# Optimization experiments

Measured on AMD Instinct MI355X. Metric: run time of the kernel, lower is better.

Reference implementation:

```python
import jax, jax.numpy as jnp
import numpy as np

D_IN = 1024
D_OUT = 1024
NUM_HEADS = 16
HEAD_DIM = D_OUT // NUM_HEADS


def setup_inputs() -> dict:
    key = jax.random.key(0)
    k_x, k_qkv, k_pw, k_pb = jax.random.split(key, 4)
    x = jax.random.normal(k_x, (2, 2048, D_IN), dtype=jnp.float32)
    # torch nn.Linear(d_in, 3*d_out, bias=False): weight [3*d_out, d_in]
    w_qkv = jax.random.normal(k_qkv, (3 * D_OUT, D_IN), dtype=jnp.float32) * (1.0 / np.sqrt(D_IN))
    # proj: nn.Linear(d_out, d_out) with bias
    w_proj = jax.random.normal(k_pw, (D_OUT, D_OUT), dtype=jnp.float32) * (1.0 / np.sqrt(D_OUT))
    b_proj = jax.random.normal(k_pb, (D_OUT,), dtype=jnp.float32) * 0.01
    return {"x": x, "w_qkv": w_qkv, "w_proj": w_proj, "b_proj": b_proj}


def reference(x, w_qkv, w_proj, b_proj):
    B, S, _ = x.shape
    # fused QKV projection: [B,S,3*D_OUT]
    qkv = jnp.einsum('bsd,ed->bse', x, w_qkv)
    qkv = qkv.reshape(B, S, 3, NUM_HEADS, HEAD_DIM)
    q, k, v = jnp.moveaxis(qkv, 2, 0)  # each [B,S,H,Dh]
    scale = 1.0 / jnp.sqrt(jnp.asarray(HEAD_DIM, dtype=x.dtype))
    # scores [B,H,S,S]
    scores = jnp.einsum('bqhd,bkhd->bhqk', q, k) * scale
    causal = jnp.tril(jnp.ones((S, S), dtype=bool))
    scores = jnp.where(causal, scores, jnp.asarray(-jnp.inf, dtype=scores.dtype))
    attn = jax.nn.softmax(scores, axis=-1)
    ctx = jnp.einsum('bhqk,bkhd->bqhd', attn, v)  # [B,S,H,Dh]
    ctx = ctx.reshape(B, S, D_OUT)
    return jnp.einsum('bsd,ed->bse', ctx, w_proj) + b_proj
```

## Files before the change

kernel.cpp:

```cpp
#include <hip/hip_runtime.h>
#include <hip/hip_bf16.h>
#include <cstdint>

#define B_SZ   2
#define S_LEN  2048
#define NH     16
#define NT     32
#define LDA    72

using f32x4 = __attribute__((ext_vector_type(4))) float;
typedef __bf16 bf16x8 __attribute__((ext_vector_type(8)));
typedef __bf16 bf16x4 __attribute__((ext_vector_type(4)));

__device__ inline float bf2f(unsigned short u) {
    union { unsigned int i; float f; } v; v.i = ((unsigned int)u) << 16; return v.f;
}
__device__ inline unsigned short f2bf(float f) {
    union { float f; unsigned int i; } v; v.f = f;
    unsigned int r = v.i + 0x7fff + ((v.i >> 16) & 1);
    return (unsigned short)(r >> 16);
}
__device__ inline f32x4 mfma16(bf16x8 a, bf16x8 b, f32x4 c) {
    return __builtin_amdgcn_mfma_f32_16x16x32_bf16(a, b, c, 0, 0, 0);
}
__device__ inline void stC(float* C, size_t idx, float v)  { C[idx] = v; }
__device__ inline void stC(__bf16* C, size_t idx, float v) { ((unsigned short*)C)[idx] = f2bf(v); }

__global__ __launch_bounds__(256) void f2b2_kernel(
    const float* __restrict__ a, int na4, __bf16* __restrict__ outa,
    const float* __restrict__ b, int nb4, __bf16* __restrict__ outb)
{
    int i = blockIdx.x * blockDim.x + threadIdx.x;
    const float* src; __bf16* dst; int idx;
    if (i < na4)           { src = a; dst = outa; idx = i; }
    else if (i < na4 + nb4){ src = b; dst = outb; idx = i - na4; }
    else return;
    float4 v = ((const float4*)src)[idx];
    ushort4 o;
    o.x = f2bf(v.x); o.y = f2bf(v.y); o.z = f2bf(v.z); o.w = f2bf(v.w);
    ((ushort4*)dst)[idx] = o;
}

__global__ __launch_bounds__(256) void f2b_kernel(
    const float* __restrict__ in, __bf16* __restrict__ out, int n4)
{
    int i = blockIdx.x * blockDim.x + threadIdx.x;
    if (i < n4) {
        float4 v = ((const float4*)in)[i];
        ushort4 o;
        o.x = f2bf(v.x); o.y = f2bf(v.y); o.z = f2bf(v.z); o.w = f2bf(v.w);
        ((ushort4*)out)[i] = o;
    }
}

template <typename TO, int HAS_BIAS>
__global__ __launch_bounds__(256) void gemm128(
    const __bf16* __restrict__ A, const __bf16* __restrict__ W,
    const float* __restrict__ bias, TO* __restrict__ C,
    int M, int N, int K)
{
    __shared__ __bf16 Alds[2][128 * 32];
    __shared__ __bf16 Blds[2][128 * 32];
    const int tid  = threadIdx.x, lane = tid & 63, w = tid >> 6;
    const int c16  = lane & 15, quad = lane >> 4;
    const int mBase = blockIdx.y * 128, nBase = blockIdx.x * 128;
    const int moff = (w & 1) * 64, noff = (w >> 1) * 64;

    f32x4 acc[4][4];
#pragma unroll
    for (int i = 0; i < 4; ++i)
#pragma unroll
        for (int j = 0; j < 4; ++j) acc[i][j] = (f32x4){0.f, 0.f, 0.f, 0.f};

    auto stage = [&](int buf, int k0) {
#pragma unroll
        for (int p = 0; p < 2; ++p) {
            const int linear = p * 256 + tid;
            const int row = linear >> 2;
            const int seg = (linear & 3) ^ (row & 3);
            const int lbase = (p * 256 + w * 64) * 8;
            const __bf16* ga = A + (size_t)(mBase + row) * K + k0 + seg * 8;
            const __bf16* gb = W + (size_t)(nBase + row) * K + k0 + seg * 8;
            __builtin_amdgcn_global_load_lds(
                (const __attribute__((address_space(1))) void*)ga,
                (__attribute__((address_space(3))) void*)(&Alds[buf][lbase]), 16, 0, 0);
            __builtin_amdgcn_global_load_lds(
                (const __attribute__((address_space(1))) void*)gb,
                (__attribute__((address_space(3))) void*)(&Blds[buf][lbase]), 16, 0, 0);
        }
    };

    stage(0, 0);
    int cur = 0;
    for (int k0 = 0; k0 < K; k0 += 32) {
        __syncthreads();
        if (k0 + 32 < K) stage(cur ^ 1, k0 + 32);

        bf16x8 af[4], bw[4];
#pragma unroll
        for (int i = 0; i < 4; ++i) {
            const int rowA = moff + i * 16 + c16;
            af[i] = *(const bf16x8*)&Alds[cur][rowA * 32 + ((quad ^ (rowA & 3)) << 3)];
            const int rowB = noff + i * 16 + c16;
            bw[i] = *(const bf16x8*)&Blds[cur][rowB * 32 + ((quad ^ (rowB & 3)) << 3)];
        }
#pragma unroll
        for (int i = 0; i < 4; ++i)
#pragma unroll
            for (int j = 0; j < 4; ++j)
                acc[i][j] = mfma16(af[i], bw[j], acc[i][j]);
        cur ^= 1;
    }

#pragma unroll
    for (int j = 0; j < 4; ++j) {
        const int col = nBase + noff + j * 16 + c16;
        const float bv = HAS_BIAS ? bias[col] : 0.f;
#pragma unroll
        for (int i = 0; i < 4; ++i)
#pragma unroll
            for (int r = 0; r < 4; ++r) {
                const int row = mBase + moff + i * 16 + quad * 4 + r;
                stC(C, (size_t)row * N + col, acc[i][j][r] + bv);
            }
    }
}

template <typename TO, int HAS_BIAS>
__global__ __launch_bounds__(256) void gemm64(
    const __bf16* __restrict__ A, const __bf16* __restrict__ W,
    const float* __restrict__ bias, TO* __restrict__ C,
    int M, int N, int K)
{
    __shared__ __bf16 Alds[2][64 * 32];
    __shared__ __bf16 Blds[2][128 * 32];
    const int tid  = threadIdx.x, lane = tid & 63, w = tid >> 6;
    const int c16  = lane & 15, quad = lane >> 4;
    const int mBase = blockIdx.y * 64, nBase = blockIdx.x * 128;
    const int moff = (w & 1) * 32, noff = (w >> 1) * 64;

    f32x4 acc[2][4];
#pragma unroll
    for (int i = 0; i < 2; ++i)
#pragma unroll
        for (int j = 0; j < 4; ++j) acc[i][j] = (f32x4){0.f, 0.f, 0.f, 0.f};

    auto stage = [&](int buf, int k0) {
        {
            const int row = tid >> 2;
            const int seg = (tid & 3) ^ (row & 3);
            const int lbase = (w * 64) * 8;
            const __bf16* ga = A + (size_t)(mBase + row) * K + k0 + seg * 8;
            __builtin_amdgcn_global_load_lds(
                (const __attribute__((address_space(1))) void*)ga,
                (__attribute__((address_space(3))) void*)(&Alds[buf][lbase]), 16, 0, 0);
        }
#pragma unroll
        for (int p = 0; p < 2; ++p) {
            const int linear = p * 256 + tid;
            const int row = linear >> 2;
            const int seg = (linear & 3) ^ (row & 3);
            const int lbase = (p * 256 + w * 64) * 8;
            const __bf16* gb = W + (size_t)(nBase + row) * K + k0 + seg * 8;
            __builtin_amdgcn_global_load_lds(
                (const __attribute__((address_space(1))) void*)gb,
                (__attribute__((address_space(3))) void*)(&Blds[buf][lbase]), 16, 0, 0);
        }
    };

    stage(0, 0);
    int cur = 0;
    for (int k0 = 0; k0 < K; k0 += 32) {
        __syncthreads();
        if (k0 + 32 < K) stage(cur ^ 1, k0 + 32);

        bf16x8 af[2], bw[4];
#pragma unroll
        for (int i = 0; i < 2; ++i) {
            const int rowA = moff + i * 16 + c16;
            af[i] = *(const bf16x8*)&Alds[cur][rowA * 32 + ((quad ^ (rowA & 3)) << 3)];
        }
#pragma unroll
        for (int j = 0; j < 4; ++j) {
            const int rowB = noff + j * 16 + c16;
            bw[j] = *(const bf16x8*)&Blds[cur][rowB * 32 + ((quad ^ (rowB & 3)) << 3)];
        }
#pragma unroll
        for (int i = 0; i < 2; ++i)
#pragma unroll
            for (int j = 0; j < 4; ++j)
                acc[i][j] = mfma16(af[i], bw[j], acc[i][j]);
        cur ^= 1;
    }

#pragma unroll
    for (int j = 0; j < 4; ++j) {
        const int col = nBase + noff + j * 16 + c16;
        const float bv = HAS_BIAS ? bias[col] : 0.f;
#pragma unroll
        for (int i = 0; i < 2; ++i)
#pragma unroll
            for (int r = 0; r < 4; ++r) {
                const int row = mBase + moff + i * 16 + quad * 4 + r;
                stC(C, (size_t)row * N + col, acc[i][j][r] + bv);
            }
    }
}

__device__ __forceinline__ void attn_tile(
    const __bf16* __restrict__ qkv, __bf16* __restrict__ ctx,
    int b, int h, int qt, int tid,
    __bf16* Qs, __bf16* Ks, __bf16* Vs, __bf16* Ps)
{
    const int lane = tid & 63;
    const int w    = tid >> 6;
    const int c16  = lane & 15;
    const int quad = lane >> 4;
    const int qBase = qt * 64;

    const float QS = 0.125f * 1.4426950408889634f;

    const int krow0 = tid >> 3;
    const int kd0   = (tid & 7) * 8;
    const int c16t = tid & 15;
    const int jh   = (tid >> 4) & 1;
    const int dblk = tid >> 5;

    const size_t rowB = (size_t)b * S_LEN;
    const __bf16* kp0 = qkv + (rowB + krow0) * 3072 + 1024 + h * 64 + kd0;
    const __bf16* kp1 = kp0 + (size_t)32 * 3072;
    const __bf16* vp0 = qkv + (rowB + 2 * jh * 16 + c16t) * 3072 + 2048 + h * 64 + dblk * 8;
    const __bf16* vp1 = vp0 + (size_t)16 * 3072;

    uint4 kr0 = *(const uint4*)kp0;
    uint4 kr1 = *(const uint4*)kp1;
    uint4 vr0 = *(const uint4*)vp0;
    uint4 vr1 = *(const uint4*)vp1;

#pragma unroll
    for (int p = 0; p < 2; ++p) {
        const int linear = p * 256 + tid;
        const int row = linear >> 3;
        const int d0 = (linear & 7) * 8;
        const __bf16* g = qkv + (rowB + qBase + row) * 3072 + h * 64 + d0;
        uint4 raw = *(const uint4*)g;
        const unsigned short* u = (const unsigned short*)&raw;
        unsigned short tmp[8];
#pragma unroll
        for (int jj = 0; jj < 8; ++jj) tmp[jj] = f2bf(bf2f(u[jj]) * QS);
        *(uint4*)&Qs[row * LDA + d0] = *(const uint4*)tmp;
    }
    __syncthreads();

    const bf16x8 aq0 = *(const bf16x8*)&Qs[(w * 16 + c16) * LDA + quad * 8];
    const bf16x8 aq1 = *(const bf16x8*)&Qs[(w * 16 + c16) * LDA + 32 + quad * 8];

    float l_r[4] = {0.f, 0.f, 0.f, 0.f};
    f32x4 acc_o[4];
#pragma unroll
    for (int j = 0; j < 4; ++j) acc_o[j] = (f32x4){0.f, 0.f, 0.f, 0.f};

    const int nCh = qt + 1;
    for (int cc = 0; cc < nCh; ++cc) {
        *(uint4*)&Ks[krow0 * LDA + kd0]        = kr0;
        *(uint4*)&Ks[(krow0 + 32) * LDA + kd0] = kr1;
        {
            const unsigned short* e1 = (const unsigned short*)&vr0;
            const unsigned short* e2 = (const unsigned short*)&vr1;
#pragma unroll
            for (int d = 0; d < 8; ++d) {
                const unsigned pack = (unsigned)e1[d] | ((unsigned)e2[d] << 16);
                *(unsigned*)&Vs[(dblk * 8 + d) * LDA + c16t * 4 + 2 * jh] = pack;
            }
        }
        __syncthreads();

        if (cc + 1 < nCh) {
            kp0 += (size_t)64 * 3072; kp1 += (size_t)64 * 3072;
            vp0 += (size_t)64 * 3072; vp1 += (size_t)64 * 3072;
            kr0 = *(const uint4*)kp0;
            kr1 = *(const uint4*)kp1;
            vr0 = *(const uint4*)vp0;
            vr1 = *(const uint4*)vp1;
        }

        f32x4 sc[4];
#pragma unroll
        for (int j = 0; j < 4; ++j) sc[j] = (f32x4){0.f, 0.f, 0.f, 0.f};
#pragma unroll
        for (int j = 0; j < 4; ++j) {
            bf16x8 bk0 = *(const bf16x8*)&Ks[(j * 16 + c16) * LDA + quad * 8];
            bf16x8 bk1 = *(const bf16x8*)&Ks[(j * 16 + c16) * LDA + 32 + quad * 8];
            sc[j] = mfma16(aq0, bk0, sc[j]);
            sc[j] = mfma16(aq1, bk1, sc[j]);
        }

        if (cc == nCh - 1) {
#pragma unroll
            for (int j = 0; j < 4; ++j) {
                const int key = cc * 64 + j * 16 + c16;
#pragma unroll
                for (int r = 0; r < 4; ++r) {
                    const int q = qBase + w * 16 + quad * 4 + r;
                    if (key > q) sc[j][r] = -1e30f;
                }
            }
        }

        float p_[4][4];
#pragma unroll
        for (int j = 0; j < 4; ++j)
#pragma unroll
            for (int r = 0; r < 4; ++r)
                p_[j][r] = exp2f(sc[j][r]);
#pragma unroll
        for (int r = 0; r < 4; ++r)
            l_r[r] += (p_[0][r] + p_[1][r]) + (p_[2][r] + p_[3][r]);

#pragma unroll
        for (int r = 0; r < 4; ++r) {
            bf16x4 pb;
            pb[0] = (__bf16)p_[0][r]; pb[1] = (__bf16)p_[1][r];
            pb[2] = (__bf16)p_[2][r]; pb[3] = (__bf16)p_[3][r];
            *(bf16x4*)&Ps[(w * 16 + quad * 4 + r) * LDA + c16 * 4] = pb;
        }

        bf16x8 ap0 = *(const bf16x8*)&Ps[(w * 16 + c16) * LDA + quad * 8];
        bf16x8 ap1 = *(const bf16x8*)&Ps[(w * 16 + c16) * LDA + 32 + quad * 8];
#pragma unroll
        for (int j = 0; j < 4; ++j) {
            bf16x8 bv0 = *(const bf16x8*)&Vs[(j * 16 + c16) * LDA + quad * 8];
            bf16x8 bv1 = *(const bf16x8*)&Vs[(j * 16 + c16) * LDA + 32 + quad * 8];
            acc_o[j] = mfma16(ap0, bv0, acc_o[j]);
            acc_o[j] = mfma16(ap1, bv1, acc_o[j]);
        }
        __syncthreads();
    }

#pragma unroll
    for (int r = 0; r < 4; ++r) {
        float l = l_r[r];
        l += __shfl_xor(l, 1);
        l += __shfl_xor(l, 2);
        l += __shfl_xor(l, 4);
        l += __shfl_xor(l, 8);
        const float inv = 1.0f / l;
        const size_t rowO = (rowB + qBase + w * 16 + quad * 4 + r) * 1024 + h * 64;
#pragma unroll
        for (int j = 0; j < 4; ++j)
            ctx[rowO + j * 16 + c16] = (__bf16)(acc_o[j][r] * inv);
    }
}

__global__ __launch_bounds__(256) void attn(
    const __bf16* __restrict__ qkv, __bf16* __restrict__ ctx)
{
    __shared__ __bf16 Qs[64 * LDA];
    __shared__ __bf16 Ks[64 * LDA];
    __shared__ __bf16 Vs[64 * LDA];
    __shared__ __bf16 Ps[64 * LDA];

    const int bh = blockIdx.x, b = bh >> 4, h = bh & 15;
    const int y  = blockIdx.y;

    attn_tile(qkv, ctx, b, h, NT - 1 - y, threadIdx.x, Qs, Ks, Vs, Ps);
    attn_tile(qkv, ctx, b, h, y,          threadIdx.x, Qs, Ks, Vs, Ps);
}

extern "C" void kernel_launch(void* const* d_in, const int* in_sizes, int n_in,
                              void* d_out, int out_size, void* d_ws, size_t ws_size,
                              hipStream_t stream) {
    const float* x      = (const float*)d_in[0];
    const float* w_qkv  = (const float*)d_in[1];
    const float* w_proj = (const float*)d_in[2];
    const float* b_proj = (const float*)d_in[3];
    float* out = (float*)d_out;

    __bf16* qkvb = (__bf16*)d_ws;
    __bf16* xb   = qkvb + (size_t)4096 * 3072;
    __bf16* wqb  = xb + (size_t)4096 * 1024;
    __bf16* ctxb = xb;
    __bf16* wpb  = wqb;

    const int M = B_SZ * S_LEN;
    const int nx4 = 4096 * 1024 / 4, nq4 = 3072 * 1024 / 4, np4 = 1024 * 1024 / 4;

    f2b2_kernel<<<(nx4 + nq4 + 255) / 256, 256, 0, stream>>>(x, nx4, xb, w_qkv, nq4, wqb);

    gemm128<__bf16, 0><<<dim3(3072 / 128, M / 128), 256, 0, stream>>>(
        xb, wqb, nullptr, qkvb, M, 3072, 1024);

    f2b_kernel<<<(np4 + 255) / 256, 256, 0, stream>>>(w_proj, wpb, np4);

    attn<<<dim3(B_SZ * NH, NT / 2), 256, 0, stream>>>(qkvb, ctxb);

    gemm64<float, 1><<<dim3(1024 / 128, M / 64), 256, 0, stream>>>(
        ctxb, wpb, b_proj, out, M, 1024, 1024);
}
```

Before: 190.9 us.

## Split long causal attention rows into two KV segments with combine kernel

```diff
diff --git a/kernel.cpp b/kernel.cpp
--- a/kernel.cpp
+++ b/kernel.cpp
@@ -207,16 +207,30 @@
     }
 }
 
-__device__ __forceinline__ void attn_tile(
+__global__ __launch_bounds__(256) void attn(
     const __bf16* __restrict__ qkv, __bf16* __restrict__ ctx,
-    int b, int h, int qt, int tid,
-    __bf16* Qs, __bf16* Ks, __bf16* Vs, __bf16* Ps)
-{
+    float* __restrict__ opart, float* __restrict__ lpart)
+{
+    __shared__ __bf16 Qs[64 * LDA];
+    __shared__ __bf16 Ks[64 * LDA];
+    __shared__ __bf16 Vs[64 * LDA];
+    __shared__ __bf16 Ps[64 * LDA];
+
+    const int tid  = threadIdx.x;
     const int lane = tid & 63;
     const int w    = tid >> 6;
     const int c16  = lane & 15;
     const int quad = lane >> 4;
+    const int bh = blockIdx.x, b = bh >> 4, h = bh & 15;
+    const int y  = blockIdx.y;
+
+    int qt, c0, c1, seg;
+    bool split;
+    if (y < 16)      { qt = 16 + y; const int half = (qt + 2) >> 1; c0 = 0;    c1 = half;   split = true;  seg = 0; }
+    else if (y < 32) { qt = y;      const int half = (qt + 2) >> 1; c0 = half; c1 = qt + 1; split = true;  seg = 1; }
+    else             { qt = 47 - y; c0 = 0; c1 = qt + 1; split = false; seg = 0; }
     const int qBase = qt * 64;
+    const int segIdx = split ? ((bh * 16 + (qt - 16)) * 2 + seg) : 0;
 
     const float QS = 0.125f * 1.4426950408889634f;
 
@@ -227,9 +241,9 @@
     const int dblk = tid >> 5;
 
     const size_t rowB = (size_t)b * S_LEN;
-    const __bf16* kp0 = qkv + (rowB + krow0) * 3072 + 1024 + h * 64 + kd0;
+    const __bf16* kp0 = qkv + (rowB + c0 * 64 + krow0) * 3072 + 1024 + h * 64 + kd0;
     const __bf16* kp1 = kp0 + (size_t)32 * 3072;
-    const __bf16* vp0 = qkv + (rowB + 2 * jh * 16 + c16t) * 3072 + 2048 + h * 64 + dblk * 8;
+    const __bf16* vp0 = qkv + (rowB + c0 * 64 + 2 * jh * 16 + c16t) * 3072 + 2048 + h * 64 + dblk * 8;
     const __bf16* vp1 = vp0 + (size_t)16 * 3072;
 
     uint4 kr0 = *(const uint4*)kp0;
@@ -260,8 +274,7 @@
 #pragma unroll
     for (int j = 0; j < 4; ++j) acc_o[j] = (f32x4){0.f, 0.f, 0.f, 0.f};
 
-    const int nCh = qt + 1;
-    for (int cc = 0; cc < nCh; ++cc) {
+    for (int cc = c0; cc < c1; ++cc) {
         *(uint4*)&Ks[krow0 * LDA + kd0]        = kr0;
         *(uint4*)&Ks[(krow0 + 32) * LDA + kd0] = kr1;
         {
@@ -275,7 +288,7 @@
         }
         __syncthreads();
 
-        if (cc + 1 < nCh) {
+        if (cc + 1 < c1) {
             kp0 += (size_t)64 * 3072; kp1 += (size_t)64 * 3072;
             vp0 += (size_t)64 * 3072; vp1 += (size_t)64 * 3072;
             kr0 = *(const uint4*)kp0;
@@ -295,7 +308,7 @@
             sc[j] = mfma16(aq1, bk1, sc[j]);
         }
 
-        if (cc == nCh - 1) {
+        if (cc == qt) {
 #pragma unroll
             for (int j = 0; j < 4; ++j) {
                 const int key = cc * 64 + j * 16 + c16;
@@ -337,34 +350,66 @@
         __syncthreads();
     }
 
-#pragma unroll
-    for (int r = 0; r < 4; ++r) {
-        float l = l_r[r];
-        l += __shfl_xor(l, 1);
-        l += __shfl_xor(l, 2);
-        l += __shfl_xor(l, 4);
-        l += __shfl_xor(l, 8);
-        const float inv = 1.0f / l;
-        const size_t rowO = (rowB + qBase + w * 16 + quad * 4 + r) * 1024 + h * 64;
-#pragma unroll
-        for (int j = 0; j < 4; ++j)
-            ctx[rowO + j * 16 + c16] = (__bf16)(acc_o[j][r] * inv);
-    }
-}
-
-__global__ __launch_bounds__(256) void attn(
-    const __bf16* __restrict__ qkv, __bf16* __restrict__ ctx)
-{
-    __shared__ __bf16 Qs[64 * LDA];
-    __shared__ __bf16 Ks[64 * LDA];
-    __shared__ __bf16 Vs[64 * LDA];
-    __shared__ __bf16 Ps[64 * LDA];
-
-    const int bh = blockIdx.x, b = bh >> 4, h = bh & 15;
-    const int y  = blockIdx.y;
-
-    attn_tile(qkv, ctx, b, h, NT - 1 - y, threadIdx.x, Qs, Ks, Vs, Ps);
-    attn_tile(qkv, ctx, b, h, y,          threadIdx.x, Qs, Ks, Vs, Ps);
+    if (!split) {
+#pragma unroll
+        for (int r = 0; r < 4; ++r) {
+            float l = l_r[r];
+            l += __shfl_xor(l, 1);
+            l += __shfl_xor(l, 2);
+            l += __shfl_xor(l, 4);
+            l += __shfl_xor(l, 8);
+            const float inv = 1.0f / l;
+            const size_t rowO = (rowB + qBase + w * 16 + quad * 4 + r) * 1024 + h * 64;
+#pragma unroll
+            for (int j = 0; j < 4; ++j)
+                ctx[rowO + j * 16 + c16] = (__bf16)(acc_o[j][r] * inv);
+        }
+    } else {
+        float* ob = opart + (size_t)segIdx * 4096;
+#pragma unroll
+        for (int r = 0; r < 4; ++r) {
+            float l = l_r[r];
+            l += __shfl_xor(l, 1);
+            l += __shfl_xor(l, 2);
+            l += __shfl_xor(l, 4);
+            l += __shfl_xor(l, 8);
+            const int qrow = w * 16 + quad * 4 + r;
+            if (c16 == 0) lpart[segIdx * 64 + qrow] = l;
+#pragma unroll
+            for (int j = 0; j < 4; ++j)
+                ob[qrow * 64 + j * 16 + c16] = acc_o[j][r];
+        }
+    }
+}
+
+__global__ __launch_bounds__(256) void attn_combine(
+    const float* __restrict__ opart, const float* __restrict__ lpart,
+    __bf16* __restrict__ ctx)
+{
+    const int blk = blockIdx.x;
+    const int bh = blk >> 4, t = blk & 15;
+    const int b = bh >> 4, h = bh & 15;
+    const int qt = 16 + t;
+    const int tid = threadIdx.x;
+    const int q  = tid >> 2;
+    const int d0 = (tid & 3) * 16;
+    const int segA = blk * 2, segB = segA + 1;
+    const float* oa = opart + (size_t)segA * 4096 + q * 64 + d0;
+    const float* obp = opart + (size_t)segB * 4096 + q * 64 + d0;
+    const float inv = 1.0f / (lpart[segA * 64 + q] + lpart[segB * 64 + q]);
+    unsigned short outv[16];
+#pragma unroll
+    for (int i = 0; i < 4; ++i) {
+        float4 a = ((const float4*)oa)[i];
+        float4 c = ((const float4*)obp)[i];
+        outv[4 * i + 0] = f2bf((a.x + c.x) * inv);
+        outv[4 * i + 1] = f2bf((a.y + c.y) * inv);
+        outv[4 * i + 2] = f2bf((a.z + c.z) * inv);
+        outv[4 * i + 3] = f2bf((a.w + c.w) * inv);
+    }
+    __bf16* dst = ctx + ((size_t)(b * S_LEN + qt * 64 + q)) * 1024 + h * 64 + d0;
+    *(uint4*)dst       = *(const uint4*)&outv[0];
+    *(uint4*)(dst + 8) = *(const uint4*)&outv[8];
 }
 
 extern "C" void kernel_launch(void* const* d_in, const int* in_sizes, int n_in,
@@ -381,6 +426,8 @@
     __bf16* wqb  = xb + (size_t)4096 * 1024;
     __bf16* ctxb = xb;
     __bf16* wpb  = wqb;
+    float*  lpart = (float*)(wqb + (size_t)1024 * 1024);
+    float* opart = out;
 
     const int M = B_SZ * S_LEN;
     const int nx4 = 4096 * 1024 / 4, nq4 = 3072 * 1024 / 4, np4 = 1024 * 1024 / 4;
@@ -392,7 +439,8 @@
 
     f2b_kernel<<<(np4 + 255) / 256, 256, 0, stream>>>(w_proj, wpb, np4);
 
-    attn<<<dim3(B_SZ * NH, NT / 2), 256, 0, stream>>>(qkvb, ctxb);
+    attn<<<dim3(B_SZ * NH, 48), 256, 0, stream>>>(qkvb, ctxb, opart, lpart);
+    attn_combine<<<B_SZ * NH * 16, 256, 0, stream>>>(opart, lpart, ctxb);
 
     gemm64<float, 1><<<dim3(1024 / 128, M / 64), 256, 0, stream>>>(
         ctxb, wpb, b_proj, out, M, 1024, 1024);
```

Result: faster. 184.9 us (-3.1%).
